# Optimization experiments

Measured on AMD Instinct MI355X. Metric: run time of the kernel, lower is better.

## Reference

```python
import jax, jax.numpy as jnp
import numpy as np

N_NODES = 10000
N_REL = 50
R_AUG = 2 * N_REL + 1  # forward + inverse + self-loop relation
D_EMB = 128
D_H1 = 128
D_H2 = 128
N_EDGES = 320000
N_BATCH = 65536


def setup_inputs() -> dict:
    key = jax.random.key(0)
    ks = jax.random.split(key, 10)
    s = jax.random.randint(ks[0], (N_EDGES,), 0, N_NODES)
    p = jax.random.randint(ks[1], (N_EDGES,), 0, N_REL)
    o = jax.random.randint(ks[2], (N_EDGES,), 0, N_NODES)
    graph = jnp.stack([s, p, o], axis=1)  # [E,3] (subject, relation, object)
    bs = jax.random.randint(ks[3], (N_BATCH,), 0, N_NODES)
    bp = jax.random.randint(ks[4], (N_BATCH,), 0, N_REL)
    bo = jax.random.randint(ks[5], (N_BATCH,), 0, N_NODES)
    batch = jnp.stack([bs, bp, bo], axis=1)  # [B,3] triples to score
    node_embeddings = jax.random.normal(ks[6], (N_NODES, D_EMB), jnp.float32) * 0.02
    W1 = jax.random.normal(ks[7], (R_AUG, D_EMB, D_H1), jnp.float32) * 0.02
    b1 = jnp.zeros((D_H1,), jnp.float32)
    W2 = jax.random.normal(ks[8], (R_AUG, D_H1, D_H2), jnp.float32) * 0.02
    b2 = jnp.zeros((D_H2,), jnp.float32)
    relations = jax.random.normal(ks[9], (N_REL, D_H2), jnp.float32) * 0.02
    return {"graph": graph, "batch": batch, "node_embeddings": node_embeddings,
            "W1": W1, "b1": b1, "W2": W2, "b2": b2, "relations": relations}


def _augment_edges(graph):
    # Add inverse relations (r + N_REL) and self-loops (relation 2*N_REL),
    # matching torch-rgcn's num_relations = nrel*2 + 1 construction.
    s, p, o = graph[:, 0], graph[:, 1], graph[:, 2]
    loop = jnp.arange(N_NODES, dtype=graph.dtype)
    src = jnp.concatenate([s, o, loop])
    rel = jnp.concatenate([p, p + N_REL, jnp.full((N_NODES,), 2 * N_REL, graph.dtype)])
    dst = jnp.concatenate([o, s, loop])
    return src, rel, dst


def _rgcn_layer(x, src, rel, dst, W, b):
    # Per-(relation, target-node) row normalization 1/c_{i,r}, then
    # h_i = sum_r W_r^T * sum_{j in N_r(i)} x_j / c_{i,r} + b
    seg = rel * N_NODES + dst  # segment id over stacked (R*N) adjacency rows
    deg = jax.ops.segment_sum(jnp.ones_like(seg, dtype=x.dtype), seg,
                              num_segments=R_AUG * N_NODES)
    norm = 1.0 / jnp.maximum(deg, 1.0)
    msg = x[src] * norm[seg][:, None]                      # [Etot, d_in]
    agg = jax.ops.segment_sum(msg, seg, num_segments=R_AUG * N_NODES)
    agg = agg.reshape(R_AUG, N_NODES, -1)                  # [R, N, d_in]
    return jnp.einsum('rnd,rdo->no', agg, W) + b           # [N, d_out]


def reference(graph, batch, node_embeddings, W1, b1, W2, b2, relations):
    src, rel, dst = _augment_edges(graph)
    x = _rgcn_layer(node_embeddings, src, rel, dst, W1, b1)
    x = jax.nn.relu(x)
    x = _rgcn_layer(x, src, rel, dst, W2, b2)
    # DistMult scoring: gather s/p/o embeddings, elementwise multiply, reduce.
    s_e = x[batch[:, 0]]
    p_e = relations[batch[:, 1]]
    o_e = x[batch[:, 2]]
    return (s_e * p_e * o_e).sum(axis=1)  # [B]
```

## Files before the change

kernel.cpp:

```cpp
#include <hip/hip_runtime.h>

#define N_NODES 10000
#define N_RELS  50
#define R_AUG   101
#define D       128
#define N_EDGES 320000
#define E_AUG   650000
#define N_BATCH 65536

#define NBINS   N_NODES
#define NSB     ((NBINS + 255) / 256)
#define NP      (R_AUG * N_NODES)
#define NPB4    ((NP + 1023) / 1024)
#define BSPAN   256
#define GEMM_NBLK (101 + (E_AUG + BSPAN - 1) / BSPAN)
#define SCAT_BLOCKS ((E_AUG + 255) / 256)

#define PREPX_BLOCKS 5000
#define TW_BLOCKS    808
#define HIST_BLOCKS  2540

typedef short bf16x8 __attribute__((ext_vector_type(8)));
typedef float f32x4  __attribute__((ext_vector_type(4)));

__device__ __forceinline__ unsigned short f2bf(float f) {
    union { float f; unsigned int u; } v; v.f = f;
    unsigned int r = (v.u + 0x7FFFu + ((v.u >> 16) & 1u)) >> 16;
    return (unsigned short)r;
}
__device__ __forceinline__ float bf2f(unsigned short h) {
    union { unsigned int u; float f; } v; v.u = ((unsigned int)h) << 16;
    return v.f;
}
__device__ __forceinline__ float u2f(unsigned int u) {
    union { unsigned int u; float f; } v; v.u = u; return v.f;
}
__device__ __forceinline__ unsigned int f2u(float f) {
    union { float f; unsigned int u; } v; v.f = f; return v.u;
}

__device__ __forceinline__ void decode_edge(const int* __restrict__ g, int e,
                                            int& src, int& rel, int& dst) {
    if (e < N_EDGES)            { src = g[3*e];     rel = g[3*e+1];          dst = g[3*e+2]; }
    else if (e < 2*N_EDGES)     { int b = e - N_EDGES;
                                  src = g[3*b+2];   rel = g[3*b+1] + N_RELS; dst = g[3*b];   }
    else                        { int n = e - 2*N_EDGES; src = n; dst = n; rel = 2*N_RELS;   }
}


__global__ __launch_bounds__(256) void prep_all(const float* __restrict__ x,
                                                unsigned short* __restrict__ xb,
                                                const float* __restrict__ W1,
                                                const float* __restrict__ W2,
                                                unsigned short* __restrict__ W1t,
                                                unsigned short* __restrict__ W2t,
                                                const int* __restrict__ g,
                                                int* __restrict__ deg,
                                                int* __restrict__ flags) {
    __shared__ float tile[64][65];
    int b = blockIdx.x, t = threadIdx.x;
    if (b < PREPX_BLOCKS) {
        int i = b * 256 + t;
        xb[i] = f2bf(x[i]);
    } else if (b < PREPX_BLOCKS + TW_BLOCKS) {
        int q = b - PREPX_BLOCKS;
        int d0 = (q & 1) * 64, o0 = ((q >> 1) & 1) * 64;
        int z = q >> 2;
        const float* W = (z < R_AUG) ? W1 : W2;
        unsigned short* Wt = (z < R_AUG) ? W1t : W2t;
        int r = (z < R_AUG) ? z : (z - R_AUG);
        int tx = t & 63, ty = t >> 6;
        #pragma unroll
        for (int i = ty; i < 64; i += 4)
            tile[i][tx] = W[((size_t)r * D + (d0 + i)) * D + (o0 + tx)];
        __syncthreads();
        #pragma unroll
        for (int i = ty; i < 64; i += 4)
            Wt[((size_t)r * D + (o0 + i)) * D + (d0 + tx)] = f2bf(tile[tx][i]);
    } else {
        int e = (b - PREPX_BLOCKS - TW_BLOCKS) * 256 + t;
        if (e < E_AUG) {
            int src, rel, dst;
            decode_edge(g, e, src, rel, dst);
            atomicAdd(&deg[rel * N_NODES + dst], 1);
            flags[rel * N_NODES + src] = 1;
        }
    }
}


__global__ __launch_bounds__(256) void scan_a(const int* __restrict__ deg,
                                              int* __restrict__ offs,
                                              int* __restrict__ part,
                                              const int* __restrict__ flags,
                                              int* __restrict__ S,
                                              int* __restrict__ ppart) {
    __shared__ int wsum[4];
    int t = threadIdx.x, lane = t & 63, w = t >> 6;
    int b = blockIdx.x;
    if (b < NSB) {
        int i = b * 256 + t;
        int v = 0;
        if (i < NBINS) {
            for (int r = 0; r < R_AUG; r++) v += deg[r * N_NODES + i];
        }
        int incl = v;
        #pragma unroll
        for (int off = 1; off < 64; off <<= 1) {
            int u = __shfl_up(incl, off, 64);
            if (lane >= off) incl += u;
        }
        if (lane == 63) wsum[w] = incl;
        __syncthreads();
        int woff = 0;
        for (int k = 0; k < w; k++) woff += wsum[k];
        if (i < NBINS) offs[i] = woff + incl - v;
        if (t == 255) part[b] = woff + incl;
    } else {
        int pb = b - NSB;
        int i0 = pb * 1024 + t * 4;
        int4 f = {0, 0, 0, 0};
        if (i0 + 3 < NP) {
            f = *(const int4*)(flags + i0);
        } else if (i0 < NP) {
            f.x = flags[i0];
            if (i0 + 1 < NP) f.y = flags[i0 + 1];
            if (i0 + 2 < NP) f.z = flags[i0 + 2];
        }
        int e1 = f.x, e2 = f.x + f.y, e3 = e2 + f.z, v = e3 + f.w;
        int incl = v;
        #pragma unroll
        for (int off = 1; off < 64; off <<= 1) {
            int u = __shfl_up(incl, off, 64);
            if (lane >= off) incl += u;
        }
        if (lane == 63) wsum[w] = incl;
        __syncthreads();
        int woff = 0;
        for (int k = 0; k < w; k++) woff += wsum[k];
        int texcl = woff + incl - v;
        if (i0 + 3 < NP) {
            int4 o = {texcl, texcl + e1, texcl + e2, texcl + e3};
            *(int4*)(S + i0) = o;
        } else if (i0 < NP) {
            S[i0] = texcl;
            if (i0 + 1 < NP) S[i0 + 1] = texcl + e1;
            if (i0 + 2 < NP) S[i0 + 2] = texcl + e2;
        }
        if (t == 255) ppart[pb] = woff + incl;
    }
}


__global__ __launch_bounds__(256) void scan_b(int* __restrict__ part,
                                              int* __restrict__ ppart,
                                              int* __restrict__ S) {
    __shared__ int wsum[4];
    int t = threadIdx.x, lane = t & 63, w = t >> 6;
    if (blockIdx.x == 0) {
        int v = (t < NSB) ? part[t] : 0;
        int incl = v;
        #pragma unroll
        for (int off = 1; off < 64; off <<= 1) {
            int u = __shfl_up(incl, off, 64);
            if (lane >= off) incl += u;
        }
        if (lane == 63) wsum[w] = incl;
        __syncthreads();
        int woff = 0;
        for (int k = 0; k < w; k++) woff += wsum[k];
        if (t < NSB) part[t] = woff + incl - v;
    } else {
        int carry = 0;
        for (int base = 0; base < NPB4; base += 256) {
            int i = base + t;
            int v = (i < NPB4) ? ppart[i] : 0;
            int incl = v;
            #pragma unroll
            for (int off = 1; off < 64; off <<= 1) {
                int u = __shfl_up(incl, off, 64);
                if (lane >= off) incl += u;
            }
            if (lane == 63) wsum[w] = incl;
            __syncthreads();
            int woff = 0;
            for (int k = 0; k < w; k++) woff += wsum[k];
            if (i < NPB4) ppart[i] = carry + woff + incl - v;
            carry += wsum[0] + wsum[1] + wsum[2] + wsum[3];
            __syncthreads();
        }
        if (t == 0) S[NP] = carry;
    }
}


__global__ __launch_bounds__(256) void scan_c(int* __restrict__ offs,
                                              const int* __restrict__ part,
                                              int* __restrict__ cursor,
                                              const int* __restrict__ flags,
                                              int* __restrict__ S,
                                              const int* __restrict__ ppart,
                                              int* __restrict__ pair_src) {
    int b = blockIdx.x, t = threadIdx.x;
    if (b < NSB) {
        int i = b * 256 + t;
        if (i < NBINS) {
            int v = offs[i] + part[i >> 8];
            offs[i] = v;
            cursor[i] = v;
        }
        if (i == 0) offs[NBINS] = E_AUG;
    } else {
        int pb = b - NSB;
        int i0 = pb * 1024 + t * 4;
        if (i0 >= NP) return;
        int pp = ppart[pb];
        if (i0 + 3 < NP) {
            int4 sv = *(int4*)(S + i0);
            sv.x += pp; sv.y += pp; sv.z += pp; sv.w += pp;
            *(int4*)(S + i0) = sv;
            int4 f = *(const int4*)(flags + i0);
            if (f.x) pair_src[sv.x] = i0 % N_NODES;
            if (f.y) pair_src[sv.y] = (i0 + 1) % N_NODES;
            if (f.z) pair_src[sv.z] = (i0 + 2) % N_NODES;
            if (f.w) pair_src[sv.w] = (i0 + 3) % N_NODES;
        } else {
            for (int k = 0; k < 4; k++) {
                int i = i0 + k;
                if (i >= NP) break;
                int s = S[i] + pp;
                S[i] = s;
                if (flags[i]) pair_src[s] = i % N_NODES;
            }
        }
    }
}

__global__ __launch_bounds__(256) void blk_kernel(const int* __restrict__ S,
                                                  int* __restrict__ rowbase,
                                                  int* __restrict__ rowcnt,
                                                  int* __restrict__ blkoffs) {
    __shared__ int wsum[4];
    int t = threadIdx.x, lane = t & 63, w = t >> 6;
    int nb = 0;
    if (t < R_AUG) {
        int base = S[t * N_NODES];
        int nxt  = S[(t + 1) * N_NODES];
        rowbase[t] = base;
        rowcnt[t]  = nxt - base;
        nb = (nxt - base + BSPAN - 1) / BSPAN;
    }
    int incl = nb;
    #pragma unroll
    for (int off = 1; off < 64; off <<= 1) {
        int u = __shfl_up(incl, off, 64);
        if (lane >= off) incl += u;
    }
    if (lane == 63) wsum[w] = incl;
    __syncthreads();
    int woff = 0;
    for (int k = 0; k < w; k++) woff += wsum[k];
    if (t < R_AUG) blkoffs[t] = woff + incl - nb;
    if (t == R_AUG) blkoffs[R_AUG] = woff + incl;
}


__global__ __launch_bounds__(256, 3) void gemm_fused(const unsigned short* __restrict__ xb,
                                                     const unsigned short* __restrict__ Wt,
                                                     const int* __restrict__ pair_src,
                                                     const int* __restrict__ rowbase,
                                                     const int* __restrict__ rowcnt,
                                                     const int* __restrict__ blkoffs,
                                                     unsigned short* __restrict__ Zc,
                                                     const int* __restrict__ g,
                                                     const int* __restrict__ deg,
                                                     const int* __restrict__ S,
                                                     int* __restrict__ cursor,
                                                     uint2* __restrict__ sorted,
                                                     int scatBlocks) {
    int b = blockIdx.x;
    int t = threadIdx.x;
    if (b < scatBlocks) {
        int e = b * 256 + t;
        if (e < E_AUG) {
            int src, rel, dst;
            decode_edge(g, e, src, rel, dst);
            int pos = atomicAdd(&cursor[dst], 1);
            int dg = deg[rel * N_NODES + dst];
            uint2 rec;
            rec.x = (unsigned)S[rel * N_NODES + src];
            rec.y = f2u(1.0f / (float)dg);
            sorted[pos] = rec;
        }
        return;
    }
    b -= scatBlocks;
    if (b >= blkoffs[R_AUG]) return;
    int lo = 0, hi = R_AUG;
    while (hi - lo > 1) {
        int mid = (lo + hi) >> 1;
        if (blkoffs[mid] <= b) lo = mid; else hi = mid;
    }
    int r = lo;
    int lb = b - blkoffs[r];
    int rbase = rowbase[r] + lb * BSPAN;
    int nrows = rowcnt[r] - lb * BSPAN; if (nrows > BSPAN) nrows = BSPAN;

    int wave = t >> 6, lane = t & 63;
    int lr = lane & 15, lq = lane >> 4;
    int no = (wave & 1) * 64;
    int tp = wave >> 1;
    const unsigned short* Wr = Wt + (size_t)r * D * D;

    int srcs[8];
    #pragma unroll
    for (int i = 0; i < 8; i++) {
        int row = (tp + 2 * i) * 16 + lr;
        srcs[i] = pair_src[rbase + (row < nrows ? row : 0)];
    }

    int prow = ((lr >> 2) << 3) + (lr & 3);
    bf16x8 w0[4], w1[4], w2[4], w3[4];
    #pragma unroll
    for (int ks = 0; ks < 4; ks++) {
        size_t kb = ks * 32 + lq * 8;
        w0[ks] = *(const bf16x8*)(Wr + (size_t)(no + prow) * D + kb);
        w1[ks] = *(const bf16x8*)(Wr + (size_t)(no + prow + 4) * D + kb);
        w2[ks] = *(const bf16x8*)(Wr + (size_t)(no + 32 + prow) * D + kb);
        w3[ks] = *(const bf16x8*)(Wr + (size_t)(no + 32 + prow + 4) * D + kb);
    }

    bf16x8 a[4];
    {
        const unsigned short* x0 = xb + (size_t)srcs[0] * D + lq * 8;
        #pragma unroll
        for (int ks = 0; ks < 4; ks++) a[ks] = *(const bf16x8*)(x0 + ks * 32);
    }

    #pragma unroll
    for (int i = 0; i < 8; i++) {
        int tile = tp + 2 * i;
        if (tile * 16 >= nrows) break;

        bf16x8 an[4];
        {
            int ni = (i < 7) ? i + 1 : 7;
            const unsigned short* xn = xb + (size_t)srcs[ni] * D + lq * 8;
            #pragma unroll
            for (int ks = 0; ks < 4; ks++) an[ks] = *(const bf16x8*)(xn + ks * 32);
        }

        f32x4 c0 = {}, c1 = {}, c2 = {}, c3 = {};
        #pragma unroll
        for (int ks = 0; ks < 4; ks++) {
            c0 = __builtin_amdgcn_mfma_f32_16x16x32_bf16(w0[ks], a[ks], c0, 0, 0, 0);
            c1 = __builtin_amdgcn_mfma_f32_16x16x32_bf16(w1[ks], a[ks], c1, 0, 0, 0);
            c2 = __builtin_amdgcn_mfma_f32_16x16x32_bf16(w2[ks], a[ks], c2, 0, 0, 0);
            c3 = __builtin_amdgcn_mfma_f32_16x16x32_bf16(w3[ks], a[ks], c3, 0, 0, 0);
        }
        int row = tile * 16 + lr;
        if (row < nrows) {
            unsigned short* zrow = Zc + ((size_t)(rbase + row) << 7);
            uint4 p0, p1;
            p0.x = (unsigned)f2bf(c0[0]) | ((unsigned)f2bf(c0[1]) << 16);
            p0.y = (unsigned)f2bf(c0[2]) | ((unsigned)f2bf(c0[3]) << 16);
            p0.z = (unsigned)f2bf(c1[0]) | ((unsigned)f2bf(c1[1]) << 16);
            p0.w = (unsigned)f2bf(c1[2]) | ((unsigned)f2bf(c1[3]) << 16);
            p1.x = (unsigned)f2bf(c2[0]) | ((unsigned)f2bf(c2[1]) << 16);
            p1.y = (unsigned)f2bf(c2[2]) | ((unsigned)f2bf(c2[3]) << 16);
            p1.z = (unsigned)f2bf(c3[0]) | ((unsigned)f2bf(c3[1]) << 16);
            p1.w = (unsigned)f2bf(c3[2]) | ((unsigned)f2bf(c3[3]) << 16);
            *(uint4*)(zrow + no + lq * 8) = p0;
            *(uint4*)(zrow + no + 32 + lq * 8) = p1;
        }
        #pragma unroll
        for (int ks = 0; ks < 4; ks++) a[ks] = an[ks];
    }
}


__global__ __launch_bounds__(256) void agg_pass(const uint2* __restrict__ sorted,
                                                const int* __restrict__ offs,
                                                const unsigned short* __restrict__ Zc,
                                                const float* __restrict__ bias,
                                                float* __restrict__ hf,
                                                unsigned short* __restrict__ hb,
                                                int dorelu) {
    int w = threadIdx.x >> 6, lane = threadIdx.x & 63;
    int dst = blockIdx.x * 4 + w;
    if (dst >= N_NODES) return;
    int e0 = offs[dst], e1 = offs[dst + 1];
    int g = lane >> 3, s = lane & 7;
    float acc[16] = {};

    for (int base = e0; base < e1; base += 64) {
        int n = e1 - base; if (n > 64) n = 64;
        uint2 rec = {0u, 0u};
        if (lane < n) rec = sorted[base + lane];
        int iters = (n + 7) >> 3;
        #pragma unroll 2
        for (int j = 0; j < iters; j++) {
            int ej = j * 8 + g;
            int ec = (ej < n) ? ej : (n - 1);
            unsigned zi = (unsigned)__shfl((int)rec.x, ec, 64);
            unsigned nb = (unsigned)__shfl((int)rec.y, ec, 64);
            float nrm = (ej < n) ? u2f(nb) : 0.0f;
            const unsigned short* zp = Zc + ((size_t)zi << 7) + s * 16;
            uint4 z0 = *(const uint4*)zp;
            uint4 z1 = *(const uint4*)(zp + 8);
            acc[0]  += nrm * bf2f((unsigned short)(z0.x & 0xFFFFu));
            acc[1]  += nrm * bf2f((unsigned short)(z0.x >> 16));
            acc[2]  += nrm * bf2f((unsigned short)(z0.y & 0xFFFFu));
            acc[3]  += nrm * bf2f((unsigned short)(z0.y >> 16));
            acc[4]  += nrm * bf2f((unsigned short)(z0.z & 0xFFFFu));
            acc[5]  += nrm * bf2f((unsigned short)(z0.z >> 16));
            acc[6]  += nrm * bf2f((unsigned short)(z0.w & 0xFFFFu));
            acc[7]  += nrm * bf2f((unsigned short)(z0.w >> 16));
            acc[8]  += nrm * bf2f((unsigned short)(z1.x & 0xFFFFu));
            acc[9]  += nrm * bf2f((unsigned short)(z1.x >> 16));
            acc[10] += nrm * bf2f((unsigned short)(z1.y & 0xFFFFu));
            acc[11] += nrm * bf2f((unsigned short)(z1.y >> 16));
            acc[12] += nrm * bf2f((unsigned short)(z1.z & 0xFFFFu));
            acc[13] += nrm * bf2f((unsigned short)(z1.z >> 16));
            acc[14] += nrm * bf2f((unsigned short)(z1.w & 0xFFFFu));
            acc[15] += nrm * bf2f((unsigned short)(z1.w >> 16));
        }
    }
    #pragma unroll
    for (int k = 0; k < 16; k++) {
        acc[k] += __shfl_down(acc[k], 8, 64);
        acc[k] += __shfl_down(acc[k], 16, 64);
        acc[k] += __shfl_down(acc[k], 32, 64);
    }
    if (g == 0) {
        const float* bp = bias + s * 16;
        float vv[16];
        #pragma unroll
        for (int k = 0; k < 16; k++) vv[k] = bp[k] + acc[k];
        if (dorelu) {
            unsigned short* hp = hb + ((size_t)dst << 7) + s * 16;
            uint4 p0, p1;
            p0.x = (unsigned)f2bf(fmaxf(vv[0], 0.0f))  | ((unsigned)f2bf(fmaxf(vv[1], 0.0f))  << 16);
            p0.y = (unsigned)f2bf(fmaxf(vv[2], 0.0f))  | ((unsigned)f2bf(fmaxf(vv[3], 0.0f))  << 16);
            p0.z = (unsigned)f2bf(fmaxf(vv[4], 0.0f))  | ((unsigned)f2bf(fmaxf(vv[5], 0.0f))  << 16);
            p0.w = (unsigned)f2bf(fmaxf(vv[6], 0.0f))  | ((unsigned)f2bf(fmaxf(vv[7], 0.0f))  << 16);
            p1.x = (unsigned)f2bf(fmaxf(vv[8], 0.0f))  | ((unsigned)f2bf(fmaxf(vv[9], 0.0f))  << 16);
            p1.y = (unsigned)f2bf(fmaxf(vv[10], 0.0f)) | ((unsigned)f2bf(fmaxf(vv[11], 0.0f)) << 16);
            p1.z = (unsigned)f2bf(fmaxf(vv[12], 0.0f)) | ((unsigned)f2bf(fmaxf(vv[13], 0.0f)) << 16);
            p1.w = (unsigned)f2bf(fmaxf(vv[14], 0.0f)) | ((unsigned)f2bf(fmaxf(vv[15], 0.0f)) << 16);
            *(uint4*)hp = p0;
            *(uint4*)(hp + 8) = p1;
        } else {
            float* hp = hf + ((size_t)dst << 7) + s * 16;
            #pragma unroll
            for (int q = 0; q < 4; q++) {
                float4 o = {vv[q * 4], vv[q * 4 + 1], vv[q * 4 + 2], vv[q * 4 + 3]};
                *(float4*)(hp + q * 4) = o;
            }
        }
    }
}


__global__ __launch_bounds__(256) void score_kernel(const int* __restrict__ batch,
                                                    const float* __restrict__ h2,
                                                    const float* __restrict__ rels,
                                                    float* __restrict__ out) {
    int t = threadIdx.x;
    int wv = t >> 6, half = (t & 63) >> 5, sl = t & 31;
    int i = blockIdx.x * 8 + wv * 2 + half;
    int bs = batch[3*i], bp = batch[3*i+1], bo = batch[3*i+2];
    float4 s = *(const float4*)(h2   + (size_t)bs * D + sl * 4);
    float4 p = *(const float4*)(rels + (size_t)bp * D + sl * 4);
    float4 o = *(const float4*)(h2   + (size_t)bo * D + sl * 4);
    float v = s.x * p.x * o.x + s.y * p.y * o.y + s.z * p.z * o.z + s.w * p.w * o.w;
    #pragma unroll
    for (int off = 16; off > 0; off >>= 1) v += __shfl_down(v, off, 32);
    if (sl == 0) out[i] = v;
}


extern "C" void kernel_launch(void* const* d_in, const int* in_sizes, int n_in,
                              void* d_out, int out_size, void* d_ws, size_t ws_size,
                              hipStream_t stream) {
    const int*   graph = (const int*)  d_in[0];
    const int*   batch = (const int*)  d_in[1];
    const float* emb   = (const float*)d_in[2];
    const float* W1    = (const float*)d_in[3];
    const float* b1    = (const float*)d_in[4];
    const float* W2    = (const float*)d_in[5];
    const float* b2    = (const float*)d_in[6];
    const float* rels  = (const float*)d_in[7];
    float* out = (float*)d_out;

    char* base = (char*)d_ws;
    size_t off = 0;
    auto take = [&](size_t bytes) -> char* {
        char* q = base + off;
        off += (bytes + 255) & ~(size_t)255;
        return q;
    };
    int*            deg     = (int*)           take((size_t)NP * 4);
    int*            flags   = (int*)           take((size_t)NP * 4);
    int*            S       = (int*)           take((size_t)(NP + 1) * 4);
    int*            pair_src= (int*)           take((size_t)E_AUG * 4);
    int*            ppart   = (int*)           take((size_t)NPB4 * 4);
    int*            rowbase = (int*)           take((size_t)(R_AUG + 1) * 4);
    int*            rowcnt  = (int*)           take((size_t)(R_AUG + 1) * 4);
    int*            blkoffs = (int*)           take((size_t)(R_AUG + 2) * 4);
    unsigned short* xb      = (unsigned short*)take((size_t)N_NODES * D * 2);
    float*          h2      = (float*)         take((size_t)N_NODES * D * 4);
    unsigned short* h1b     = (unsigned short*)take((size_t)N_NODES * D * 2);
    unsigned short* W1t     = (unsigned short*)take((size_t)R_AUG * D * D * 2);
    unsigned short* W2t     = (unsigned short*)take((size_t)R_AUG * D * D * 2);
    int*            offs    = (int*)           take((size_t)(NBINS + 1) * 4);
    int*            cursor  = (int*)           take((size_t)NBINS * 4);
    int*            part    = (int*)           take((size_t)NSB * 4);
    uint2*          sorted  = (uint2*)         take((size_t)E_AUG * 8);
    unsigned short* Zc      = (unsigned short*)take((size_t)E_AUG * D * 2);

    hipMemsetAsync(deg, 0, (size_t)((char*)S - (char*)deg), stream);
    prep_all<<<dim3(PREPX_BLOCKS + TW_BLOCKS + HIST_BLOCKS), 256, 0, stream>>>(
        emb, xb, W1, W2, W1t, W2t, graph, deg, flags);
    scan_a<<<dim3(NSB + NPB4), 256, 0, stream>>>(deg, offs, part, flags, S, ppart);
    scan_b<<<dim3(2), 256, 0, stream>>>(part, ppart, S);
    scan_c<<<dim3(NSB + NPB4), 256, 0, stream>>>(offs, part, cursor, flags, S, ppart, pair_src);
    blk_kernel<<<dim3(1), 256, 0, stream>>>(S, rowbase, rowcnt, blkoffs);

    gemm_fused<<<dim3(SCAT_BLOCKS + GEMM_NBLK), 256, 0, stream>>>(
        xb, W1t, pair_src, rowbase, rowcnt, blkoffs, Zc,
        graph, deg, S, cursor, sorted, SCAT_BLOCKS);
    agg_pass<<<dim3((N_NODES + 3) / 4), 256, 0, stream>>>(sorted, offs, Zc, b1, (float*)0, h1b, 1);
    gemm_fused<<<dim3(GEMM_NBLK), 256, 0, stream>>>(
        h1b, W2t, pair_src, rowbase, rowcnt, blkoffs, Zc,
        graph, deg, S, cursor, sorted, 0);
    agg_pass<<<dim3((N_NODES + 3) / 4), 256, 0, stream>>>(sorted, offs, Zc, b2, h2, (unsigned short*)0, 0);
    score_kernel<<<dim3(N_BATCH / 8), 256, 0, stream>>>(batch, h2, rels, out);
}
```

Measured before the change: 342.9 us.

## Derive source-pair flags from degree of paired relation and regroup scatter kernel

Drops the separate flags array by noting that (rel, src) is used exactly when the inverse relation has a positive in-degree at that node, so the scans read deg of the paired relation instead. This removes the scattered flag stores in the histogram pass and the memset of the flags buffer. The edge scatter moves out of the layer-1 GEMM launch into its own kernel, which also absorbs the single-block row/block offset computation, so one launch is removed. The cost is that scatter no longer overlaps with the first GEMM in a single grid.

```diff
diff --git a/kernel.cpp b/kernel.cpp
--- a/kernel.cpp
+++ b/kernel.cpp
@@ -47,6 +47,10 @@
     else                        { int n = e - 2*N_EDGES; src = n; dst = n; rel = 2*N_RELS;   }
 }
 
+__device__ __forceinline__ int pair_rel(int r) {
+    return (r < N_RELS) ? r + N_RELS : (r < 2 * N_RELS ? r - N_RELS : r);
+}
+
 
 __global__ __launch_bounds__(256) void prep_all(const float* __restrict__ x,
                                                 unsigned short* __restrict__ xb,
@@ -55,8 +59,7 @@
                                                 unsigned short* __restrict__ W1t,
                                                 unsigned short* __restrict__ W2t,
                                                 const int* __restrict__ g,
-                                                int* __restrict__ deg,
-                                                int* __restrict__ flags) {
+                                                int* __restrict__ deg) {
     __shared__ float tile[64][65];
     int b = blockIdx.x, t = threadIdx.x;
     if (b < PREPX_BLOCKS) {
@@ -83,7 +86,6 @@
             int src, rel, dst;
             decode_edge(g, e, src, rel, dst);
             atomicAdd(&deg[rel * N_NODES + dst], 1);
-            flags[rel * N_NODES + src] = 1;
         }
     }
 }
@@ -92,7 +94,6 @@
 __global__ __launch_bounds__(256) void scan_a(const int* __restrict__ deg,
                                               int* __restrict__ offs,
                                               int* __restrict__ part,
-                                              const int* __restrict__ flags,
                                               int* __restrict__ S,
                                               int* __restrict__ ppart) {
     __shared__ int wsum[4];
@@ -120,12 +121,18 @@
         int pb = b - NSB;
         int i0 = pb * 1024 + t * 4;
         int4 f = {0, 0, 0, 0};
-        if (i0 + 3 < NP) {
-            f = *(const int4*)(flags + i0);
-        } else if (i0 < NP) {
-            f.x = flags[i0];
-            if (i0 + 1 < NP) f.y = flags[i0 + 1];
-            if (i0 + 2 < NP) f.z = flags[i0 + 2];
+        if (i0 < NP) {
+            int r = i0 / N_NODES;
+            int xx = i0 - r * N_NODES;
+            const int* dp = deg + pair_rel(r) * N_NODES + xx;
+            if (i0 + 3 < NP) {
+                int4 d = *(const int4*)dp;
+                f.x = d.x > 0; f.y = d.y > 0; f.z = d.z > 0; f.w = d.w > 0;
+            } else {
+                f.x = dp[0] > 0;
+                if (i0 + 1 < NP) f.y = dp[1] > 0;
+                if (i0 + 2 < NP) f.z = dp[2] > 0;
+            }
         }
         int e1 = f.x, e2 = f.x + f.y, e3 = e2 + f.z, v = e3 + f.w;
         int incl = v;
@@ -197,7 +204,7 @@
 __global__ __launch_bounds__(256) void scan_c(int* __restrict__ offs,
                                               const int* __restrict__ part,
                                               int* __restrict__ cursor,
-                                              const int* __restrict__ flags,
+                                              const int* __restrict__ deg,
                                               int* __restrict__ S,
                                               const int* __restrict__ ppart,
                                               int* __restrict__ pair_src) {
@@ -215,86 +222,86 @@
         int i0 = pb * 1024 + t * 4;
         if (i0 >= NP) return;
         int pp = ppart[pb];
+        int r = i0 / N_NODES;
+        int xx = i0 - r * N_NODES;
+        const int* dp = deg + pair_rel(r) * N_NODES + xx;
         if (i0 + 3 < NP) {
             int4 sv = *(int4*)(S + i0);
             sv.x += pp; sv.y += pp; sv.z += pp; sv.w += pp;
             *(int4*)(S + i0) = sv;
-            int4 f = *(const int4*)(flags + i0);
-            if (f.x) pair_src[sv.x] = i0 % N_NODES;
-            if (f.y) pair_src[sv.y] = (i0 + 1) % N_NODES;
-            if (f.z) pair_src[sv.z] = (i0 + 2) % N_NODES;
-            if (f.w) pair_src[sv.w] = (i0 + 3) % N_NODES;
+            int4 d = *(const int4*)dp;
+            if (d.x > 0) pair_src[sv.x] = xx;
+            if (d.y > 0) pair_src[sv.y] = xx + 1;
+            if (d.z > 0) pair_src[sv.z] = xx + 2;
+            if (d.w > 0) pair_src[sv.w] = xx + 3;
         } else {
             for (int k = 0; k < 4; k++) {
                 int i = i0 + k;
                 if (i >= NP) break;
                 int s = S[i] + pp;
                 S[i] = s;
-                if (flags[i]) pair_src[s] = i % N_NODES;
+                if (dp[k] > 0) pair_src[s] = xx + k;
             }
         }
     }
 }
 
-__global__ __launch_bounds__(256) void blk_kernel(const int* __restrict__ S,
-                                                  int* __restrict__ rowbase,
-                                                  int* __restrict__ rowcnt,
-                                                  int* __restrict__ blkoffs) {
-    __shared__ int wsum[4];
-    int t = threadIdx.x, lane = t & 63, w = t >> 6;
-    int nb = 0;
-    if (t < R_AUG) {
-        int base = S[t * N_NODES];
-        int nxt  = S[(t + 1) * N_NODES];
-        rowbase[t] = base;
-        rowcnt[t]  = nxt - base;
-        nb = (nxt - base + BSPAN - 1) / BSPAN;
-    }
-    int incl = nb;
-    #pragma unroll
-    for (int off = 1; off < 64; off <<= 1) {
-        int u = __shfl_up(incl, off, 64);
-        if (lane >= off) incl += u;
-    }
-    if (lane == 63) wsum[w] = incl;
-    __syncthreads();
-    int woff = 0;
-    for (int k = 0; k < w; k++) woff += wsum[k];
-    if (t < R_AUG) blkoffs[t] = woff + incl - nb;
-    if (t == R_AUG) blkoffs[R_AUG] = woff + incl;
-}
-
-
-__global__ __launch_bounds__(256, 3) void gemm_fused(const unsigned short* __restrict__ xb,
-                                                     const unsigned short* __restrict__ Wt,
-                                                     const int* __restrict__ pair_src,
-                                                     const int* __restrict__ rowbase,
-                                                     const int* __restrict__ rowcnt,
-                                                     const int* __restrict__ blkoffs,
-                                                     unsigned short* __restrict__ Zc,
-                                                     const int* __restrict__ g,
-                                                     const int* __restrict__ deg,
-                                                     const int* __restrict__ S,
-                                                     int* __restrict__ cursor,
-                                                     uint2* __restrict__ sorted,
-                                                     int scatBlocks) {
+
+__global__ __launch_bounds__(256) void scatter_blk(const int* __restrict__ g,
+                                                   const int* __restrict__ deg,
+                                                   const int* __restrict__ S,
+                                                   int* __restrict__ cursor,
+                                                   uint2* __restrict__ sorted,
+                                                   int* __restrict__ rowbase,
+                                                   int* __restrict__ rowcnt,
+                                                   int* __restrict__ blkoffs) {
+    int b = blockIdx.x, t = threadIdx.x;
+    if (b == 0) {
+        __shared__ int wsum[4];
+        int lane = t & 63, w = t >> 6;
+        int nb = 0;
+        if (t < R_AUG) {
+            int base = S[t * N_NODES];
+            int nxt  = S[(t + 1) * N_NODES];
+            rowbase[t] = base;
+            rowcnt[t]  = nxt - base;
+            nb = (nxt - base + BSPAN - 1) / BSPAN;
+        }
+        int incl = nb;
+        #pragma unroll
+        for (int off = 1; off < 64; off <<= 1) {
+            int u = __shfl_up(incl, off, 64);
+            if (lane >= off) incl += u;
+        }
+        if (lane == 63) wsum[w] = incl;
+        __syncthreads();
+        int woff = 0;
+        for (int k = 0; k < w; k++) woff += wsum[k];
+        if (t < R_AUG) blkoffs[t] = woff + incl - nb;
+        if (t == R_AUG) blkoffs[R_AUG] = woff + incl;
+        return;
+    }
+    int e = (b - 1) * 256 + t;
+    if (e >= E_AUG) return;
+    int src, rel, dst;
+    decode_edge(g, e, src, rel, dst);
+    int pos = atomicAdd(&cursor[dst], 1);
+    int dg = deg[rel * N_NODES + dst];
+    uint2 rec;
+    rec.x = (unsigned)S[rel * N_NODES + src];
+    rec.y = f2u(1.0f / (float)dg);
+    sorted[pos] = rec;
+}
+
+
+__global__ __launch_bounds__(256, 3) void gemm_compact(const unsigned short* __restrict__ xb,
+                                                       const unsigned short* __restrict__ Wt,
+                                                       const int* __restrict__ pair_src,
+                                                       const int* __restrict__ rowbase,
+                                                       const int* __restrict__ rowcnt,
+                                                       const int* __restrict__ blkoffs,
+                                                       unsigned short* __restrict__ Zc) {
     int b = blockIdx.x;
-    int t = threadIdx.x;
-    if (b < scatBlocks) {
-        int e = b * 256 + t;
-        if (e < E_AUG) {
-            int src, rel, dst;
-            decode_edge(g, e, src, rel, dst);
-            int pos = atomicAdd(&cursor[dst], 1);
-            int dg = deg[rel * N_NODES + dst];
-            uint2 rec;
-            rec.x = (unsigned)S[rel * N_NODES + src];
-            rec.y = f2u(1.0f / (float)dg);
-            sorted[pos] = rec;
-        }
-        return;
-    }
-    b -= scatBlocks;
     if (b >= blkoffs[R_AUG]) return;
     int lo = 0, hi = R_AUG;
     while (hi - lo > 1) {
@@ -306,7 +313,7 @@
     int rbase = rowbase[r] + lb * BSPAN;
     int nrows = rowcnt[r] - lb * BSPAN; if (nrows > BSPAN) nrows = BSPAN;
 
-    int wave = t >> 6, lane = t & 63;
+    int t = threadIdx.x, wave = t >> 6, lane = t & 63;
     int lr = lane & 15, lq = lane >> 4;
     int no = (wave & 1) * 64;
     int tp = wave >> 1;
@@ -501,7 +508,6 @@
         return q;
     };
     int*            deg     = (int*)           take((size_t)NP * 4);
-    int*            flags   = (int*)           take((size_t)NP * 4);
     int*            S       = (int*)           take((size_t)(NP + 1) * 4);
     int*            pair_src= (int*)           take((size_t)E_AUG * 4);
     int*            ppart   = (int*)           take((size_t)NPB4 * 4);
@@ -519,21 +525,18 @@
     uint2*          sorted  = (uint2*)         take((size_t)E_AUG * 8);
     unsigned short* Zc      = (unsigned short*)take((size_t)E_AUG * D * 2);
 
-    hipMemsetAsync(deg, 0, (size_t)((char*)S - (char*)deg), stream);
+    hipMemsetAsync(deg, 0, (size_t)NP * 4, stream);
     prep_all<<<dim3(PREPX_BLOCKS + TW_BLOCKS + HIST_BLOCKS), 256, 0, stream>>>(
-        emb, xb, W1, W2, W1t, W2t, graph, deg, flags);
-    scan_a<<<dim3(NSB + NPB4), 256, 0, stream>>>(deg, offs, part, flags, S, ppart);
+        emb, xb, W1, W2, W1t, W2t, graph, deg);
+    scan_a<<<dim3(NSB + NPB4), 256, 0, stream>>>(deg, offs, part, S, ppart);
     scan_b<<<dim3(2), 256, 0, stream>>>(part, ppart, S);
-    scan_c<<<dim3(NSB + NPB4), 256, 0, stream>>>(offs, part, cursor, flags, S, ppart, pair_src);
-    blk_kernel<<<dim3(1), 256, 0, stream>>>(S, rowbase, rowcnt, blkoffs);
-
-    gemm_fused<<<dim3(SCAT_BLOCKS + GEMM_NBLK), 256, 0, stream>>>(
-        xb, W1t, pair_src, rowbase, rowcnt, blkoffs, Zc,
-        graph, deg, S, cursor, sorted, SCAT_BLOCKS);
+    scan_c<<<dim3(NSB + NPB4), 256, 0, stream>>>(offs, part, cursor, deg, S, ppart, pair_src);
+    scatter_blk<<<dim3(1 + SCAT_BLOCKS), 256, 0, stream>>>(
+        graph, deg, S, cursor, sorted, rowbase, rowcnt, blkoffs);
+
+    gemm_compact<<<dim3(GEMM_NBLK), 256, 0, stream>>>(xb, W1t, pair_src, rowbase, rowcnt, blkoffs, Zc);
     agg_pass<<<dim3((N_NODES + 3) / 4), 256, 0, stream>>>(sorted, offs, Zc, b1, (float*)0, h1b, 1);
-    gemm_fused<<<dim3(GEMM_NBLK), 256, 0, stream>>>(
-        h1b, W2t, pair_src, rowbase, rowcnt, blkoffs, Zc,
-        graph, deg, S, cursor, sorted, 0);
+    gemm_compact<<<dim3(GEMM_NBLK), 256, 0, stream>>>(h1b, W2t, pair_src, rowbase, rowcnt, blkoffs, Zc);
     agg_pass<<<dim3((N_NODES + 3) / 4), 256, 0, stream>>>(sorted, offs, Zc, b2, h2, (unsigned short*)0, 0);
     score_kernel<<<dim3(N_BATCH / 8), 256, 0, stream>>>(batch, h2, rels, out);
 }
```

New measurement: 342.8 us. Within noise of the previous version (-0.0%).
